# Kernel optimization log

Measured on AMD Instinct MI355X. Metric: run time of the kernel, lower is better.

The kernel has to match this reference:

```python
import jax, jax.numpy as jnp
import numpy as np

N_NODES = 200000   # total graph nodes (var + constraint)
N_VAR   = 112000   # nodes with x[:,0]==1, placed first for static slicing
N_EDGES = 3200000  # avg degree 16
HID     = 64
BATCH   = 64       # fc output width == batch_size in the torch module
TW      = 8        # target_width; TW*(TW-1)=56; N_VAR = seq_len*56 with seq_len=2000


def setup_inputs() -> dict:
    key = jax.random.key(0)
    ks = jax.random.split(key, 8)
    x = jax.random.normal(ks[0], (N_NODES, 2), jnp.float32)
    # var_mask = (x[:,0] == 1): make the first N_VAR nodes variable nodes.
    x = x.at[:, 0].set(jnp.where(jnp.arange(N_NODES) < N_VAR, 1.0, 0.0))
    edge_index = jax.random.randint(ks[1], (2, N_EDGES), 0, N_NODES, jnp.int32)
    W1 = jax.random.normal(ks[2], (2, HID), jnp.float32) / np.sqrt(2.0)
    b1 = jnp.zeros((HID,), jnp.float32)
    W2 = jax.random.normal(ks[3], (HID, HID), jnp.float32) / np.sqrt(HID)
    b2 = jnp.zeros((HID,), jnp.float32)
    Wfc = jax.random.normal(ks[4], (HID, BATCH), jnp.float32) / np.sqrt(HID)
    bfc = jnp.zeros((BATCH,), jnp.float32)
    return {"x": x, "edge_index": edge_index, "W1": W1, "b1": b1,
            "W2": W2, "b2": b2, "Wfc": Wfc, "bfc": bfc}


def gcn_conv(x, src, dst, W, b):
    """PyG GCNConv: transform, then sym-normalized aggregation with self-loops."""
    h = x @ W                                   # [N, F_out]
    ones = jnp.ones(src.shape[0], x.dtype)
    deg = jax.ops.segment_sum(ones, dst, num_segments=N_NODES) + 1.0  # +1: self-loop
    dinv = jax.lax.rsqrt(deg)                   # deg >= 1, always safe
    norm = dinv[src] * dinv[dst]                # [E]
    agg = jax.ops.segment_sum(h[src] * norm[:, None], dst, num_segments=N_NODES)
    agg = agg + h * (dinv * dinv)[:, None]      # self-loop message, norm = dinv_i^2
    return agg + b


def reference(x, edge_index, W1, b1, W2, b2, Wfc, bfc):
    src, dst = edge_index[0], edge_index[1]
    h = jax.nn.relu(gcn_conv(x, src, dst, W1, b1))
    h = gcn_conv(h, src, dst, W2, b2)
    # var_mask == first N_VAR rows by construction (static slice for jit)
    out = jax.nn.relu(h[:N_VAR] @ Wfc + bfc)    # [N_VAR, BATCH]
    width = TW * (TW - 1)                       # 56
    seq_len = N_VAR // width                    # 2000
    return jnp.round(out.reshape(seq_len, BATCH, width))
```

## Files before the change

kernel.cpp:

```cpp
#include <hip/hip_runtime.h>
#include <math.h>

#define N_NODES 200000
#define N_VAR   112000
#define N_EDGES 3200000
#define NB_SCAN 782
#define CAP     64

#define NFINE    512
#define PSZ_F    391
#define FCAP     7168
#define BIN_CHUNK 8192
#define NB_BIN   391

typedef int v4i __attribute__((ext_vector_type(4)));

__global__ void __launch_bounds__(512) k_bin(const int* __restrict__ src,
                                             const int* __restrict__ dst,
                                             int* __restrict__ bins,
                                             int* __restrict__ bcnt,
                                             const float* __restrict__ W2,
                                             const float* __restrict__ b2,
                                             const float* __restrict__ Wfc,
                                             const float* __restrict__ bfc,
                                             float* __restrict__ Wc,
                                             float* __restrict__ bc) {
    __shared__ int hist[NFINE];
    __shared__ int seg[NFINE];
    __shared__ int gb[NFINE];
    __shared__ int cur[NFINE];
    __shared__ int wsum[8];
    __shared__ int stg[BIN_CHUNK];
    __shared__ unsigned short stgb[BIN_CHUNK];
    int tid = threadIdx.x;
    int lane = tid & 63, wid = tid >> 6;
    hist[tid] = 0;
    __syncthreads();

    int base = blockIdx.x * BIN_CHUNK;
    int pk[4][4];
    int bk[4][4];
    bool val[4];
    #pragma unroll
    for (int i = 0; i < 4; ++i) {
        int e4 = base + (i * 512 + tid) * 4;
        val[i] = (e4 < N_EDGES);
        if (val[i]) {
            v4i d = __builtin_nontemporal_load((const v4i*)(dst + e4));
            v4i s = __builtin_nontemporal_load((const v4i*)(src + e4));
            int dd[4] = {d.x, d.y, d.z, d.w};
            int ss[4] = {s.x, s.y, s.z, s.w};
            #pragma unroll
            for (int q = 0; q < 4; ++q) {
                int bb2 = dd[q] / PSZ_F;
                int dl = dd[q] - bb2 * PSZ_F;
                pk[i][q] = (dl << 18) | ss[q];
                bk[i][q] = bb2;
                atomicAdd(&hist[bb2], 1);
            }
        }
    }
    __syncthreads();

    int h = hist[tid];
    int inc = h;
    #pragma unroll
    for (int d = 1; d < 64; d <<= 1) {
        int t = __shfl_up(inc, d);
        if (lane >= d) inc += t;
    }
    if (lane == 63) wsum[wid] = inc;
    __syncthreads();
    int pre = 0, tot = 0;
    #pragma unroll
    for (int k = 0; k < 8; ++k) {
        int s = wsum[k];
        pre += (k < wid) ? s : 0;
        tot += s;
    }
    int ex = pre + inc - h;
    seg[tid] = ex;
    cur[tid] = ex;
    gb[tid]  = atomicAdd(&bcnt[tid], h);
    __syncthreads();

    #pragma unroll
    for (int i = 0; i < 4; ++i) {
        if (val[i]) {
            #pragma unroll
            for (int q = 0; q < 4; ++q) {
                int p = atomicAdd(&cur[bk[i][q]], 1);
                stg[p]  = pk[i][q];
                stgb[p] = (unsigned short)bk[i][q];
            }
        }
    }
    __syncthreads();

    for (int i = tid; i < tot; i += 512) {
        int bb2 = stgb[i];
        int pos = gb[bb2] + (i - seg[bb2]);
        if (pos < FCAP)
            bins[(size_t)bb2 * FCAP + pos] = stg[i];
    }

    int b = blockIdx.x;
    if (b < 8) {
        int e = b * 512 + tid;
        int j = e >> 6, l2 = e & 63;
        double acc = 0.0;
        for (int m = 0; m < 64; ++m)
            acc += (double)W2[j * 64 + m] * (double)Wfc[m * 64 + l2];
        Wc[e] = (float)acc;
    } else if (b == 8 && tid < 64) {
        double acc = (double)bfc[tid];
        for (int m = 0; m < 64; ++m)
            acc += (double)b2[m] * (double)Wfc[m * 64 + tid];
        bc[tid] = (float)acc;
    }
}

__global__ void __launch_bounds__(512) k_sort(const int* __restrict__ bins,
                                              const int* __restrict__ bcnt,
                                              const float2* __restrict__ x2,
                                              int* __restrict__ cnt,
                                              float4* __restrict__ xdc,
                                              int* __restrict__ buf) {
    __shared__ int hist[NFINE];
    __shared__ int off[NFINE];
    __shared__ int cur[NFINE];
    __shared__ int wsum[8];
    __shared__ int sorted[FCAP];
    __shared__ unsigned short rowid[FCAP];
    int tid = threadIdx.x;
    int lane = tid & 63, wid = tid >> 6;
    int b = blockIdx.x;
    int n = bcnt[b];
    if (n > FCAP) n = FCAP;
    const int* __restrict__ bp = bins + (size_t)b * FCAP;

    hist[tid] = 0;
    __syncthreads();
    for (int i = tid; i < n; i += 512)
        atomicAdd(&hist[bp[i] >> 18], 1);
    __syncthreads();

    int h = hist[tid];

    int vg = b * PSZ_F + tid;
    if (tid < PSZ_F && vg < N_NODES) {
        cnt[vg] = h;
        float dvv = rsqrtf((float)h + 1.0f);
        float2 xv = x2[vg];
        xdc[vg] = make_float4(xv.x * dvv, xv.y * dvv, dvv, 0.0f);
    }

    int inc = h;
    #pragma unroll
    for (int d = 1; d < 64; d <<= 1) {
        int t = __shfl_up(inc, d);
        if (lane >= d) inc += t;
    }
    if (lane == 63) wsum[wid] = inc;
    __syncthreads();
    int pre = 0;
    #pragma unroll
    for (int k = 0; k < 8; ++k) {
        int s = wsum[k];
        pre += (k < wid) ? s : 0;
    }
    int ex = pre + inc - h;
    off[tid] = ex;
    cur[tid] = ex;
    __syncthreads();

    for (int i = tid; i < n; i += 512) {
        int pkv = bp[i];
        int dl = pkv >> 18;
        int p = atomicAdd(&cur[dl], 1);
        sorted[p] = pkv & 0x3FFFF;
        rowid[p]  = (unsigned short)dl;
    }
    __syncthreads();

    for (int i = tid; i < n; i += 512) {
        int dl = rowid[i];
        int slot = i - off[dl];
        if (slot < CAP)
            buf[(size_t)(b * PSZ_F + dl) * CAP + slot] = sorted[i];
    }
}

__global__ void __launch_bounds__(256) k_l1a(const int* __restrict__ cnt,
                                             const int* __restrict__ buf,
                                             const float4* __restrict__ xdc,
                                             float4* __restrict__ zn) {
    int v = blockIdx.x * 256 + threadIdx.x;
    if (v >= N_NODES) return;
    int c = cnt[v];
    int n = (c < CAP) ? c : CAP;
    const int* __restrict__ rowp = buf + v * CAP;
    float4 self = xdc[v];
    float dv = self.z;
    float ax = self.x, ay = self.y;
    float bx = 0.0f,   by = 0.0f;
    int j = 0;
    for (; j + 16 <= n; j += 16) {
        v4i r0 = __builtin_nontemporal_load((const v4i*)(rowp + j));
        v4i r1 = __builtin_nontemporal_load((const v4i*)(rowp + j + 4));
        v4i r2 = __builtin_nontemporal_load((const v4i*)(rowp + j + 8));
        v4i r3 = __builtin_nontemporal_load((const v4i*)(rowp + j + 12));
        float4 p0 = xdc[r0.x], p1 = xdc[r0.y], p2 = xdc[r0.z], p3 = xdc[r0.w];
        float4 p4 = xdc[r1.x], p5 = xdc[r1.y], p6 = xdc[r1.z], p7 = xdc[r1.w];
        float4 p8 = xdc[r2.x], p9 = xdc[r2.y], pa = xdc[r2.z], pb = xdc[r2.w];
        float4 pc = xdc[r3.x], pd = xdc[r3.y], pe = xdc[r3.z], pf = xdc[r3.w];
        ax += p0.x; ay += p0.y;  bx += p1.x; by += p1.y;
        ax += p2.x; ay += p2.y;  bx += p3.x; by += p3.y;
        ax += p4.x; ay += p4.y;  bx += p5.x; by += p5.y;
        ax += p6.x; ay += p6.y;  bx += p7.x; by += p7.y;
        ax += p8.x; ay += p8.y;  bx += p9.x; by += p9.y;
        ax += pa.x; ay += pa.y;  bx += pb.x; by += pb.y;
        ax += pc.x; ay += pc.y;  bx += pd.x; by += pd.y;
        ax += pe.x; ay += pe.y;  bx += pf.x; by += pf.y;
    }
    for (; j + 8 <= n; j += 8) {
        v4i r0 = __builtin_nontemporal_load((const v4i*)(rowp + j));
        v4i r1 = __builtin_nontemporal_load((const v4i*)(rowp + j + 4));
        float4 p0 = xdc[r0.x], p1 = xdc[r0.y], p2 = xdc[r0.z], p3 = xdc[r0.w];
        float4 p4 = xdc[r1.x], p5 = xdc[r1.y], p6 = xdc[r1.z], p7 = xdc[r1.w];
        ax += p0.x; ay += p0.y;  bx += p1.x; by += p1.y;
        ax += p2.x; ay += p2.y;  bx += p3.x; by += p3.y;
        ax += p4.x; ay += p4.y;  bx += p5.x; by += p5.y;
        ax += p6.x; ay += p6.y;  bx += p7.x; by += p7.y;
    }
    for (; j < n; ++j) {
        int s = rowp[j];
        float4 p = xdc[s];
        ax += p.x; ay += p.y;
    }
    zn[v] = make_float4((ax + bx) * dv, (ay + by) * dv, dv, 0.0f);
}

__global__ void __launch_bounds__(256, 4) k_l2(const int* __restrict__ cnt,
                                               const int* __restrict__ buf,
                                               const float4* __restrict__ zn,
                                               const float* __restrict__ W1,
                                               const float* __restrict__ b1,
                                               const float* __restrict__ Wc,
                                               const float* __restrict__ bc,
                                               float* __restrict__ out) {
    __shared__ __align__(16) float4 pb[4][64];
    __shared__ __align__(16) float  avs[4][64];
    int w = threadIdx.x >> 6, l = threadIdx.x & 63;
    float4* __restrict__ pbw = &pb[w][0];
    float*  __restrict__ avw = &avs[w][0];
    float wc[64];
    #pragma unroll
    for (int jv = 0; jv < 64; ++jv)
        wc[jv] = Wc[jv * 64 + l];
    float w1a = W1[l], w1b = W1[64 + l], bb = b1[l];
    float bcl = bc[l];
    int v0 = blockIdx.x * 16 + w;
    int cc0 = __builtin_amdgcn_readfirstlane(cnt[v0]);
    int cc1 = __builtin_amdgcn_readfirstlane(cnt[v0 + 4]);
    int cc2 = __builtin_amdgcn_readfirstlane(cnt[v0 + 8]);
    int cc3 = __builtin_amdgcn_readfirstlane(cnt[v0 + 12]);

    int nn[4];
    float4 p[4], zs[4];
    #pragma unroll
    for (int it = 0; it < 4; ++it) {
        int v = v0 + it * 4;
        int c = (it == 0) ? cc0 : (it == 1) ? cc1 : (it == 2) ? cc2 : cc3;
        int n = (c < CAP) ? c : CAP;
        nn[it] = n;
        int ridx = __builtin_nontemporal_load(buf + v * CAP + l);
        int idx  = (l < n) ? ridx : v;
        p[it]  = zn[idx];
        zs[it] = zn[v];
    }

    #pragma unroll
    for (int it = 0; it < 4; ++it) {
        int v = v0 + it * 4;
        int c = (it == 0) ? cc0 : (it == 1) ? cc1 : (it == 2) ? cc2 : cc3;
        int n = nn[it];
        float dv = rsqrtf((float)c + 1.0f);
        float4 zss = zs[it];

        pbw[l] = p[it];

        float acc0 = fmaxf(fmaf(zss.x, w1a, fmaf(zss.y, w1b, bb)), 0.0f) * zss.z;
        float acc1 = 0.0f;
        int j = 0;
        for (; j + 8 <= n; j += 8) {
            float4 q0 = pbw[j+0], q1 = pbw[j+1], q2 = pbw[j+2], q3 = pbw[j+3];
            float4 q4 = pbw[j+4], q5 = pbw[j+5], q6 = pbw[j+6], q7 = pbw[j+7];
            float h0 = fmaxf(fmaf(q0.x, w1a, fmaf(q0.y, w1b, bb)), 0.0f) * q0.z;
            float h1 = fmaxf(fmaf(q1.x, w1a, fmaf(q1.y, w1b, bb)), 0.0f) * q1.z;
            float h2 = fmaxf(fmaf(q2.x, w1a, fmaf(q2.y, w1b, bb)), 0.0f) * q2.z;
            float h3 = fmaxf(fmaf(q3.x, w1a, fmaf(q3.y, w1b, bb)), 0.0f) * q3.z;
            float h4 = fmaxf(fmaf(q4.x, w1a, fmaf(q4.y, w1b, bb)), 0.0f) * q4.z;
            float h5 = fmaxf(fmaf(q5.x, w1a, fmaf(q5.y, w1b, bb)), 0.0f) * q5.z;
            float h6 = fmaxf(fmaf(q6.x, w1a, fmaf(q6.y, w1b, bb)), 0.0f) * q6.z;
            float h7 = fmaxf(fmaf(q7.x, w1a, fmaf(q7.y, w1b, bb)), 0.0f) * q7.z;
            acc0 += (h0 + h1) + (h2 + h3);
            acc1 += (h4 + h5) + (h6 + h7);
        }
        for (; j + 4 <= n; j += 4) {
            float4 q0 = pbw[j+0], q1 = pbw[j+1], q2 = pbw[j+2], q3 = pbw[j+3];
            float h0 = fmaxf(fmaf(q0.x, w1a, fmaf(q0.y, w1b, bb)), 0.0f) * q0.z;
            float h1 = fmaxf(fmaf(q1.x, w1a, fmaf(q1.y, w1b, bb)), 0.0f) * q1.z;
            float h2 = fmaxf(fmaf(q2.x, w1a, fmaf(q2.y, w1b, bb)), 0.0f) * q2.z;
            float h3 = fmaxf(fmaf(q3.x, w1a, fmaf(q3.y, w1b, bb)), 0.0f) * q3.z;
            acc0 += (h0 + h1) + (h2 + h3);
        }
        for (; j < n; ++j) {
            float4 q0 = pbw[j];
            acc1 += fmaxf(fmaf(q0.x, w1a, fmaf(q0.y, w1b, bb)), 0.0f) * q0.z;
        }
        float Av = (acc0 + acc1) * dv;

        avw[l] = Av;

        float t0 = 0.0f, t1 = 0.0f, t2 = 0.0f, t3 = 0.0f;
        #pragma unroll
        for (int jj = 0; jj < 64; jj += 4) {
            float4 a4 = *(const float4*)&avw[jj];
            t0 = fmaf(a4.x, wc[jj + 0], t0);
            t1 = fmaf(a4.y, wc[jj + 1], t1);
            t2 = fmaf(a4.z, wc[jj + 2], t2);
            t3 = fmaf(a4.w, wc[jj + 3], t3);
        }
        float t = ((t0 + t1) + (t2 + t3)) + bcl;
        __builtin_nontemporal_store(rintf(fmaxf(t, 0.0f)), out + v * 64 + l);
    }
}


extern "C" void kernel_launch(void* const* d_in, const int* in_sizes, int n_in,
                              void* d_out, int out_size, void* d_ws, size_t ws_size,
                              hipStream_t stream) {
    const float* x    = (const float*)d_in[0];
    const int*   ei   = (const int*)  d_in[1];
    const float* W1   = (const float*)d_in[2];
    const float* b1   = (const float*)d_in[3];
    const float* W2   = (const float*)d_in[4];
    const float* b2   = (const float*)d_in[5];
    const float* Wfc  = (const float*)d_in[6];
    const float* bfc  = (const float*)d_in[7];
    float* out = (float*)d_out;

    const int* src = ei;
    const int* dst = ei + N_EDGES;

    char* ws = (char*)d_ws;
    int*    cnt    = (int*)   (ws + 0);
    float4* xdc    = (float4*)(ws + 800000);
    int*    bins   = (int*)   (ws + 4000000);
    int*    bcnt   = (int*)   (ws + 18680064);
    float4* zn     = (float4*)(ws + 15204096);
    int*    buf    = (int*)   (ws + 19204096);
    float*  Wc     = (float*) (ws + 70404096);
    float*  bc     = (float*) (ws + 70420480);

    hipMemsetAsync(bcnt, 0, NFINE * sizeof(int), stream);
    k_bin  <<<NB_BIN, 512, 0, stream>>>(src, dst, bins, bcnt, W2, b2, Wfc, bfc, Wc, bc);
    k_sort <<<NFINE, 512, 0, stream>>>(bins, bcnt, (const float2*)x, cnt, xdc, buf);
    k_l1a  <<<NB_SCAN, 256, 0, stream>>>(cnt, buf, xdc, zn);
    k_l2   <<<N_VAR / 16, 256, 0, stream>>>(cnt, buf, zn, W1, b1, Wc, bc, out);
}
```

Measured before the change: 206.1 us.

## Process layer-1 aggregation with one wavefront per node and LDS reduction

```diff
diff --git a/kernel.cpp b/kernel.cpp
--- a/kernel.cpp
+++ b/kernel.cpp
@@ -4,7 +4,6 @@
 #define N_NODES 200000
 #define N_VAR   112000
 #define N_EDGES 3200000
-#define NB_SCAN 782
 #define CAP     64
 
 #define NFINE    512
@@ -12,6 +11,7 @@
 #define FCAP     7168
 #define BIN_CHUNK 8192
 #define NB_BIN   391
+#define NB_L1    12500
 
 typedef int v4i __attribute__((ext_vector_type(4)));
 
@@ -191,54 +191,80 @@
     }
 }
 
-__global__ void __launch_bounds__(256) k_l1a(const int* __restrict__ cnt,
-                                             const int* __restrict__ buf,
-                                             const float4* __restrict__ xdc,
-                                             float4* __restrict__ zn) {
-    int v = blockIdx.x * 256 + threadIdx.x;
-    if (v >= N_NODES) return;
-    int c = cnt[v];
-    int n = (c < CAP) ? c : CAP;
-    const int* __restrict__ rowp = buf + v * CAP;
-    float4 self = xdc[v];
-    float dv = self.z;
-    float ax = self.x, ay = self.y;
-    float bx = 0.0f,   by = 0.0f;
-    int j = 0;
-    for (; j + 16 <= n; j += 16) {
-        v4i r0 = __builtin_nontemporal_load((const v4i*)(rowp + j));
-        v4i r1 = __builtin_nontemporal_load((const v4i*)(rowp + j + 4));
-        v4i r2 = __builtin_nontemporal_load((const v4i*)(rowp + j + 8));
-        v4i r3 = __builtin_nontemporal_load((const v4i*)(rowp + j + 12));
-        float4 p0 = xdc[r0.x], p1 = xdc[r0.y], p2 = xdc[r0.z], p3 = xdc[r0.w];
-        float4 p4 = xdc[r1.x], p5 = xdc[r1.y], p6 = xdc[r1.z], p7 = xdc[r1.w];
-        float4 p8 = xdc[r2.x], p9 = xdc[r2.y], pa = xdc[r2.z], pb = xdc[r2.w];
-        float4 pc = xdc[r3.x], pd = xdc[r3.y], pe = xdc[r3.z], pf = xdc[r3.w];
-        ax += p0.x; ay += p0.y;  bx += p1.x; by += p1.y;
-        ax += p2.x; ay += p2.y;  bx += p3.x; by += p3.y;
-        ax += p4.x; ay += p4.y;  bx += p5.x; by += p5.y;
-        ax += p6.x; ay += p6.y;  bx += p7.x; by += p7.y;
-        ax += p8.x; ay += p8.y;  bx += p9.x; by += p9.y;
-        ax += pa.x; ay += pa.y;  bx += pb.x; by += pb.y;
-        ax += pc.x; ay += pc.y;  bx += pd.x; by += pd.y;
-        ax += pe.x; ay += pe.y;  bx += pf.x; by += pf.y;
-    }
-    for (; j + 8 <= n; j += 8) {
-        v4i r0 = __builtin_nontemporal_load((const v4i*)(rowp + j));
-        v4i r1 = __builtin_nontemporal_load((const v4i*)(rowp + j + 4));
-        float4 p0 = xdc[r0.x], p1 = xdc[r0.y], p2 = xdc[r0.z], p3 = xdc[r0.w];
-        float4 p4 = xdc[r1.x], p5 = xdc[r1.y], p6 = xdc[r1.z], p7 = xdc[r1.w];
-        ax += p0.x; ay += p0.y;  bx += p1.x; by += p1.y;
-        ax += p2.x; ay += p2.y;  bx += p3.x; by += p3.y;
-        ax += p4.x; ay += p4.y;  bx += p5.x; by += p5.y;
-        ax += p6.x; ay += p6.y;  bx += p7.x; by += p7.y;
-    }
-    for (; j < n; ++j) {
-        int s = rowp[j];
-        float4 p = xdc[s];
-        ax += p.x; ay += p.y;
-    }
-    zn[v] = make_float4((ax + bx) * dv, (ay + by) * dv, dv, 0.0f);
+__global__ void __launch_bounds__(256, 4) k_l1a(const int* __restrict__ cnt,
+                                                const int* __restrict__ buf,
+                                                const float4* __restrict__ xdc,
+                                                float4* __restrict__ zn) {
+    __shared__ __align__(16) float2 pb2[4][64];
+    int w = threadIdx.x >> 6, l = threadIdx.x & 63;
+    float2* __restrict__ pbw = &pb2[w][0];
+    int v0 = blockIdx.x * 16 + w;
+    int cc0 = __builtin_amdgcn_readfirstlane(cnt[v0]);
+    int cc1 = __builtin_amdgcn_readfirstlane(cnt[v0 + 4]);
+    int cc2 = __builtin_amdgcn_readfirstlane(cnt[v0 + 8]);
+    int cc3 = __builtin_amdgcn_readfirstlane(cnt[v0 + 12]);
+
+    int nn[4];
+    float2 g[4];
+    float4 zs[4];
+    #pragma unroll
+    for (int it = 0; it < 4; ++it) {
+        int v = v0 + it * 4;
+        int c = (it == 0) ? cc0 : (it == 1) ? cc1 : (it == 2) ? cc2 : cc3;
+        int n = (c < CAP) ? c : CAP;
+        nn[it] = n;
+        int ridx = __builtin_nontemporal_load(buf + v * CAP + l);
+        int idx  = (l < n) ? ridx : v;
+        g[it]  = *(const float2*)&xdc[idx];
+        zs[it] = xdc[v];
+    }
+
+    #pragma unroll
+    for (int it = 0; it < 4; ++it) {
+        int v = v0 + it * 4;
+        int n = nn[it];
+        float4 self = zs[it];
+        float dv = self.z;
+        pbw[l] = g[it];
+
+        float ax = self.x, ay = self.y;
+        float bx = 0.0f,   by = 0.0f;
+        int j = 0;
+        for (; j + 16 <= n; j += 16) {
+            float4 q0 = *(const float4*)&pbw[j +  0];
+            float4 q1 = *(const float4*)&pbw[j +  2];
+            float4 q2 = *(const float4*)&pbw[j +  4];
+            float4 q3 = *(const float4*)&pbw[j +  6];
+            float4 q4 = *(const float4*)&pbw[j +  8];
+            float4 q5 = *(const float4*)&pbw[j + 10];
+            float4 q6 = *(const float4*)&pbw[j + 12];
+            float4 q7 = *(const float4*)&pbw[j + 14];
+            ax += q0.x; ay += q0.y;  bx += q0.z; by += q0.w;
+            ax += q1.x; ay += q1.y;  bx += q1.z; by += q1.w;
+            ax += q2.x; ay += q2.y;  bx += q2.z; by += q2.w;
+            ax += q3.x; ay += q3.y;  bx += q3.z; by += q3.w;
+            ax += q4.x; ay += q4.y;  bx += q4.z; by += q4.w;
+            ax += q5.x; ay += q5.y;  bx += q5.z; by += q5.w;
+            ax += q6.x; ay += q6.y;  bx += q6.z; by += q6.w;
+            ax += q7.x; ay += q7.y;  bx += q7.z; by += q7.w;
+        }
+        for (; j + 8 <= n; j += 8) {
+            float4 q0 = *(const float4*)&pbw[j + 0];
+            float4 q1 = *(const float4*)&pbw[j + 2];
+            float4 q2 = *(const float4*)&pbw[j + 4];
+            float4 q3 = *(const float4*)&pbw[j + 6];
+            ax += q0.x; ay += q0.y;  bx += q0.z; by += q0.w;
+            ax += q1.x; ay += q1.y;  bx += q1.z; by += q1.w;
+            ax += q2.x; ay += q2.y;  bx += q2.z; by += q2.w;
+            ax += q3.x; ay += q3.y;  bx += q3.z; by += q3.w;
+        }
+        for (; j < n; ++j) {
+            float2 q = pbw[j];
+            ax += q.x; ay += q.y;
+        }
+        if (l == 0)
+            zn[v] = make_float4((ax + bx) * dv, (ay + by) * dv, dv, 0.0f);
+    }
 }
 
 __global__ void __launch_bounds__(256, 4) k_l2(const int* __restrict__ cnt,
@@ -367,6 +393,6 @@
     hipMemsetAsync(bcnt, 0, NFINE * sizeof(int), stream);
     k_bin  <<<NB_BIN, 512, 0, stream>>>(src, dst, bins, bcnt, W2, b2, Wfc, bfc, Wc, bc);
     k_sort <<<NFINE, 512, 0, stream>>>(bins, bcnt, (const float2*)x, cnt, xdc, buf);
-    k_l1a  <<<NB_SCAN, 256, 0, stream>>>(cnt, buf, xdc, zn);
+    k_l1a  <<<NB_L1, 256, 0, stream>>>(cnt, buf, xdc, zn);
     k_l2   <<<N_VAR / 16, 256, 0, stream>>>(cnt, buf, zn, W1, b1, Wc, bc, out);
 }
```

After: 198.8 us. -3.5%, faster.
